# Kernel optimization log

Hardware: AMD Instinct MI355X
Metric: run time of the kernel (lower is better)

Reference implementation:

```python
import jax, jax.numpy as jnp
import numpy as np

N, E = 50000, 800000
NODE_IN, EDGE_IN, HID, OUT = 64, 16, 64, 32
BN_EPS = 1e-5


def _linear_params(key, fan_in, fan_out):
    kw, kb = jax.random.split(key)
    lim = 1.0 / np.sqrt(fan_in)
    W = jax.random.uniform(kw, (fan_in, fan_out), minval=-lim, maxval=lim, dtype=jnp.float32)
    b = jax.random.uniform(kb, (fan_out,), minval=-lim, maxval=lim, dtype=jnp.float32)
    return W, b


def setup_inputs() -> dict:
    key = jax.random.key(0)
    ks = jax.random.split(key, 8)
    x = jax.random.normal(ks[0], (N, NODE_IN), dtype=jnp.float32)
    edge_index = jax.random.randint(ks[1], (2, E), 0, N, dtype=jnp.int64)
    edge_attr = jax.random.normal(ks[2], (E, EDGE_IN), dtype=jnp.float32)
    # layer 1: message Linear(node_in + edge_in -> hid), self Linear(node_in -> hid)
    W1_msg, b1_msg = _linear_params(ks[3], NODE_IN + EDGE_IN, HID)
    W1_self, b1_self = _linear_params(ks[4], NODE_IN, HID)
    # BatchNorm1d(hidden) params (inference mode: running stats)
    bn_gamma = jnp.ones((HID,), jnp.float32)
    bn_beta = jnp.zeros((HID,), jnp.float32)
    bn_mean = jax.random.normal(ks[5], (HID,), dtype=jnp.float32) * 0.1
    bn_var = jax.random.uniform(ks[6], (HID,), minval=0.5, maxval=1.5, dtype=jnp.float32)
    # layer 2: message Linear(hid + edge_in -> out), self Linear(hid -> out)
    k7, k8 = jax.random.split(ks[7])
    W2_msg, b2_msg = _linear_params(k7, HID + EDGE_IN, OUT)
    W2_self, b2_self = _linear_params(k8, HID, OUT)
    return dict(x=x, edge_index=edge_index, edge_attr=edge_attr,
                W1_msg=W1_msg, b1_msg=b1_msg, W1_self=W1_self, b1_self=b1_self,
                bn_gamma=bn_gamma, bn_beta=bn_beta, bn_mean=bn_mean, bn_var=bn_var,
                W2_msg=W2_msg, b2_msg=b2_msg, W2_self=W2_self, b2_self=b2_self)


def _gnn_layer(x, edge_index, edge_attr, W_msg, b_msg, W_self, b_self):
    # gather source node features per edge, concat edge features, linear, scatter-sum to dst
    src, dst = edge_index[0], edge_index[1]
    m = jnp.concatenate([x[src], edge_attr], axis=-1) @ W_msg + b_msg  # [E, out]
    agg = jax.ops.segment_sum(m, dst, num_segments=x.shape[0])          # [N, out]
    return x @ W_self + b_self + agg


def reference(x, edge_index, edge_attr,
              W1_msg, b1_msg, W1_self, b1_self,
              bn_gamma, bn_beta, bn_mean, bn_var,
              W2_msg, b2_msg, W2_self, b2_self):
    h = _gnn_layer(x, edge_index, edge_attr, W1_msg, b1_msg, W1_self, b1_self)
    # BatchNorm1d (eval mode, running stats) + ReLU; dropout is identity in eval
    h = (h - bn_mean) * jax.lax.rsqrt(bn_var + BN_EPS) * bn_gamma + bn_beta
    h = jax.nn.relu(h)
    return _gnn_layer(h, edge_index, edge_attr, W2_msg, b2_msg, W2_self, b2_self)
```

## Files before the change

### kernel.cpp

```cpp
#include <hip/hip_runtime.h>

#define NN 50000
#define NE 800000
#define NB 6250
#define NT 3125
#define SCB 49
#define NBK 128
#define BNODE 391
#define BCAP 7680
#define SCAP 56

typedef __attribute__((ext_vector_type(8))) short short8x;
typedef __attribute__((ext_vector_type(4))) float f32x4;

#define OFF_CNT   0LL
#define OFF_ROW   ((long long)NN)
#define OFF_RECS  (3LL*NN + 16)
#define OFF_FLAGS (35LL*NN + 16)
#define OFF_BS    (35LL*NN + 32)
#define OFF_BO    (35LL*NN + 96)
#define OFF_PK    (35LL*NN + 160)
#define OFF_FB1S  (35LL*NN + 7840)
#define OFF_FB2S  (35LL*NN + 7904)
#define OFF_F1    (36LL*NN)
#define OFF_F2    (116LL*NN)
#define OFF_Y2B   (164LL*NN)
#define OFF_S2    (180LL*NN)
#define OFF_BCUR  (212LL*NN)

__device__ __forceinline__ float ldf(const void* p, long long i, int bf16) {
  if (bf16) {
    unsigned short u = ((const unsigned short*)p)[i];
    return __uint_as_float(((unsigned)u) << 16);
  }
  return ((const float*)p)[i];
}
__device__ __forceinline__ unsigned short f2bf(float f) {
  unsigned u = __float_as_uint(f);
  unsigned r = (u + 0x7fffu + ((u >> 16) & 1u)) >> 16;
  return (unsigned short)r;
}
__device__ __forceinline__ unsigned pk2(float lo, float hi) {
  return (unsigned)f2bf(lo) | ((unsigned)f2bf(hi) << 16);
}
__device__ __forceinline__ int ldidx(const void* p, long long i, int i64) {
  return i64 ? (int)((const long long*)p)[i] : ((const int*)p)[i];
}
__device__ __forceinline__ float bflo(unsigned u) { return __uint_as_float(u << 16); }
__device__ __forceinline__ float bfhi(unsigned u) { return __uint_as_float(u & 0xffff0000u); }

__global__ void k_detect(const void* ei, const void* x, int* flags) {
  int lane = threadIdx.x & 63;
  const int* p = (const int*)ei;
  int any = 0;
  for (int i = lane; i < 256; i += 64) any |= p[2 * i + 1];
  unsigned long long anyb = __ballot(any != 0);
  const unsigned short* q = (const unsigned short*)x;
  int cnt = 0;
  for (int i = lane; i < 256; i += 64) {
    unsigned short w = q[2 * i];
    int e = (w >> 7) & 0xff;
    if (w == 0 || (e >= 110 && e <= 140)) cnt++;
  }
  for (int m = 1; m < 64; m <<= 1) cnt += __shfl_xor(cnt, m, 64);
  if (lane == 0) {
    flags[0] = (anyb == 0ull) ? 1 : 0;
    flags[1] = (cnt >= 192) ? 1 : 0;
  }
}

__global__ __launch_bounds__(256) void k_prep(
    const void* __restrict__ W1_msg, const void* __restrict__ b1_msg,
    const void* __restrict__ W1_self, const void* __restrict__ b1_self,
    const void* __restrict__ gamma, const void* __restrict__ beta,
    const void* __restrict__ mean, const void* __restrict__ var,
    const void* __restrict__ W2_msg, const void* __restrict__ b2_msg,
    const void* __restrict__ W2_self, const void* __restrict__ b2_self,
    const int* __restrict__ flags, unsigned short* __restrict__ PK,
    float* __restrict__ fb1s, float* __restrict__ fb2s) {
  int bf = flags[1];
  int t0 = blockIdx.x * 256 + threadIdx.x;
  int stride = gridDim.x * 256;
  for (int i = t0; i < 10240; i += stride) {
    int j = i & 7, L = (i >> 3) & 63, t = (i >> 9) & 3, c = i >> 11;
    int k = c * 32 + ((L >> 4) << 3) + j;
    int col = t * 16 + (L & 15);
    float sc = ldf(gamma, col, bf) * rsqrtf(ldf(var, col, bf) + 1e-5f);
    float v;
    if (k < 64) v = ldf(W1_msg, k * 64 + col, bf) * sc;
    else if (k < 128) v = ldf(W1_self, (k - 64) * 64 + col, bf) * sc;
    else if (k < 144) v = ldf(W1_msg, (64 + k - 128) * 64 + col, bf) * sc;
    else if (k == 144) v = ldf(b1_msg, col, bf) * sc;
    else v = 0.0f;
    PK[i] = f2bf(v);
  }
  for (int i = t0; i < 2048; i += stride) {
    int j = i & 7, L = (i >> 3) & 63, t = (i >> 9) & 1, c = i >> 10;
    int k = c * 32 + ((L >> 4) << 3) + j;
    int col = t * 16 + (L & 15);
    PK[10240 + i] = f2bf(ldf(W2_msg, k * 32 + col, bf));
  }
  for (int i = t0; i < 3072; i += stride) {
    int j = i & 7, L = (i >> 3) & 63, t = (i >> 9) & 1, c = i >> 10;
    int k = c * 32 + ((L >> 4) << 3) + j;
    int col = t * 16 + (L & 15);
    float v;
    if (k < 64) v = ldf(W2_self, k * 32 + col, bf);
    else if (k < 80) v = ldf(W2_msg, k * 32 + col, bf);
    else if (k == 80) v = ldf(b2_msg, col, bf);
    else v = 0.0f;
    PK[12288 + i] = f2bf(v);
  }
  for (int i = t0; i < 64; i += stride) {
    float sc = ldf(gamma, i, bf) * rsqrtf(ldf(var, i, bf) + 1e-5f);
    fb1s[i] = ldf(b1_self, i, bf) * sc + ldf(beta, i, bf) - ldf(mean, i, bf) * sc;
  }
  for (int i = t0; i < 32; i += stride) fb2s[i] = ldf(b2_self, i, bf);
}

__global__ __launch_bounds__(256) void k_bin(const void* __restrict__ ei,
                                             const int* __restrict__ flags,
                                             int* __restrict__ bcur,
                                             int2* __restrict__ binbuf) {
  __shared__ int2 stage[NBK][SCAP];
  __shared__ int scnt[NBK];
  __shared__ int gbase[NBK];
  int tid = threadIdx.x;
  for (int i = tid; i < NBK; i += 256) scnt[i] = 0;
  __syncthreads();
  int i64 = flags[0];
  for (long long e0 = (long long)blockIdx.x * 256; e0 < NE;
       e0 += (long long)gridDim.x * 256) {
    long long e = e0 + tid;
    if (e < NE) {
      int src = ldidx(ei, e, i64);
      int dst = ldidx(ei, NE + e, i64);
      int b = dst / BNODE;
      int dl = dst - b * BNODE;
      int2 ent = make_int2(src | (dl << 16), (int)e);
      int pos = atomicAdd(&scnt[b], 1);
      if (pos < SCAP) {
        stage[b][pos] = ent;
      } else {
        int gp = atomicAdd(&bcur[b], 1);
        binbuf[(long long)b * BCAP + gp] = ent;
      }
    }
  }
  __syncthreads();
  if (tid < NBK) {
    int cb = scnt[tid] < SCAP ? scnt[tid] : SCAP;
    gbase[tid] = atomicAdd(&bcur[tid], cb);
  }
  __syncthreads();
  for (int b = 0; b < NBK; ++b) {
    int cb = scnt[b] < SCAP ? scnt[b] : SCAP;
    for (int i = tid; i < cb; i += 256)
      binbuf[(long long)b * BCAP + gbase[b] + i] = stage[b][i];
  }
}

__global__ __launch_bounds__(256) void k_bhist(const int* __restrict__ bcur,
                                               const int2* __restrict__ binbuf,
                                               int* __restrict__ counts) {
  __shared__ int lh[BNODE];
  int b = blockIdx.x;
  int tid = threadIdx.x;
  for (int i = tid; i < BNODE; i += 256) lh[i] = 0;
  __syncthreads();
  int cnt = bcur[b];
  for (int i = tid; i < cnt; i += 256) {
    int dl = (binbuf[(long long)b * BCAP + i].x >> 16) & 0x3FF;
    atomicAdd(&lh[dl], 1);
  }
  __syncthreads();
  int base = b * BNODE;
  int nn = NN - base < BNODE ? NN - base : BNODE;
  for (int i = tid; i < nn; i += 256) counts[base + i] = lh[i];
}

__global__ __launch_bounds__(1024) void k_scanA(const int* __restrict__ counts,
                                                int* __restrict__ bs) {
  __shared__ int sd[1024];
  int t = threadIdx.x;
  int i = blockIdx.x * 1024 + t;
  sd[t] = (i < NN) ? counts[i] : 0;
  __syncthreads();
  for (int off = 512; off > 0; off >>= 1) {
    if (t < off) sd[t] += sd[t + off];
    __syncthreads();
  }
  if (t == 0) bs[blockIdx.x] = sd[0];
}

__global__ void k_scanB(const int* __restrict__ bs, int* __restrict__ bo) {
  int lane = threadIdx.x & 63;
  int v = (lane < SCB) ? bs[lane] : 0;
  int orig = v;
  for (int off = 1; off < 64; off <<= 1) {
    int u = __shfl_up(v, off, 64);
    if (lane >= off) v += u;
  }
  if (lane < SCB) bo[lane] = v - orig;
}

__global__ __launch_bounds__(1024) void k_scanC(const int* __restrict__ counts,
                                                const int* __restrict__ bo,
                                                int* __restrict__ row_ptr) {
  __shared__ int sd[1024];
  int t = threadIdx.x;
  int i = blockIdx.x * 1024 + t;
  int v = (i < NN) ? counts[i] : 0;
  sd[t] = v;
  __syncthreads();
  for (int off = 1; off < 1024; off <<= 1) {
    int u = (t >= off) ? sd[t - off] : 0;
    __syncthreads();
    sd[t] += u;
    __syncthreads();
  }
  int excl = sd[t] - v + bo[blockIdx.x];
  if (i < NN) row_ptr[i] = excl;
  if (i == NN - 1) row_ptr[NN] = excl + v;
}

__global__ __launch_bounds__(256) void k_place(const int* __restrict__ bcur,
                                               const int2* __restrict__ binbuf,
                                               const int* __restrict__ row_ptr,
                                               int2* __restrict__ recs) {
  __shared__ int2 outb[BCAP];
  __shared__ int lcur[BNODE];
  int b = blockIdx.x;
  int tid = threadIdx.x;
  int base = b * BNODE;
  int nn = NN - base < BNODE ? NN - base : BNODE;
  int rbase = row_ptr[base];
  for (int i = tid; i < nn; i += 256) lcur[i] = row_ptr[base + i] - rbase;
  __syncthreads();
  int cnt = bcur[b];
  for (int i = tid; i < cnt; i += 256) {
    int2 ent = binbuf[(long long)b * BCAP + i];
    int dl = (ent.x >> 16) & 0x3FF;
    int p = atomicAdd(&lcur[dl], 1);
    outb[p] = make_int2(ent.x & 0xFFFF, ent.y);
  }
  __syncthreads();
  for (int i = tid; i < cnt; i += 256) recs[rbase + i] = outb[i];
}

__global__ __launch_bounds__(256) void k_gather1(
    const void* __restrict__ x, const void* __restrict__ ea,
    const int* __restrict__ row_ptr, const int2* __restrict__ recs,
    const int* __restrict__ flags, unsigned short* __restrict__ F1,
    unsigned short* __restrict__ F2) {
  int lane = threadIdx.x & 63;
  int g = lane >> 3, c = lane & 7;
  int bf = flags[1];
  long long wid = ((long long)blockIdx.x * blockDim.x + threadIdx.x) >> 6;
  long long nw = ((long long)gridDim.x * blockDim.x) >> 6;
  for (long long b = wid; b < NB; b += nw) {
    int n = (int)(b * 8 + g);
    int beg = row_ptr[n];
    int deg = row_ptr[n + 1] - beg;
    float a0 = 0.f, a1 = 0.f, a2 = 0.f, a3 = 0.f, a4 = 0.f, a5 = 0.f, a6 = 0.f, a7 = 0.f;
    float e0 = 0.f, e1 = 0.f, e2 = 0.f, e3 = 0.f;
    uint4 xw;
    if (bf) {
      const unsigned short* xs = (const unsigned short*)x;
      const unsigned short* es = (const unsigned short*)ea;
      int t = 0;
      for (; t + 4 <= deg; t += 4) {
        int2 r0 = recs[beg + t + 0];
        int2 r1 = recs[beg + t + 1];
        int2 r2 = recs[beg + t + 2];
        int2 r3 = recs[beg + t + 3];
        uint4 w0 = *((const uint4*)(xs + ((long long)r0.x << 6)) + c);
        uint4 w1 = *((const uint4*)(xs + ((long long)r1.x << 6)) + c);
        uint4 w2 = *((const uint4*)(xs + ((long long)r2.x << 6)) + c);
        uint4 w3 = *((const uint4*)(xs + ((long long)r3.x << 6)) + c);
        a0 += bflo(w0.x) + bflo(w1.x) + bflo(w2.x) + bflo(w3.x);
        a1 += bfhi(w0.x) + bfhi(w1.x) + bfhi(w2.x) + bfhi(w3.x);
        a2 += bflo(w0.y) + bflo(w1.y) + bflo(w2.y) + bflo(w3.y);
        a3 += bfhi(w0.y) + bfhi(w1.y) + bfhi(w2.y) + bfhi(w3.y);
        a4 += bflo(w0.z) + bflo(w1.z) + bflo(w2.z) + bflo(w3.z);
        a5 += bfhi(w0.z) + bfhi(w1.z) + bfhi(w2.z) + bfhi(w3.z);
        a6 += bflo(w0.w) + bflo(w1.w) + bflo(w2.w) + bflo(w3.w);
        a7 += bfhi(w0.w) + bfhi(w1.w) + bfhi(w2.w) + bfhi(w3.w);
        if (c < 4) {
          uint2 q0 = *((const uint2*)(es + ((long long)r0.y << 4)) + c);
          uint2 q1 = *((const uint2*)(es + ((long long)r1.y << 4)) + c);
          uint2 q2 = *((const uint2*)(es + ((long long)r2.y << 4)) + c);
          uint2 q3 = *((const uint2*)(es + ((long long)r3.y << 4)) + c);
          e0 += bflo(q0.x) + bflo(q1.x) + bflo(q2.x) + bflo(q3.x);
          e1 += bfhi(q0.x) + bfhi(q1.x) + bfhi(q2.x) + bfhi(q3.x);
          e2 += bflo(q0.y) + bflo(q1.y) + bflo(q2.y) + bflo(q3.y);
          e3 += bfhi(q0.y) + bfhi(q1.y) + bfhi(q2.y) + bfhi(q3.y);
        }
      }
      for (; t < deg; ++t) {
        int2 r = recs[beg + t];
        uint4 w = *((const uint4*)(xs + ((long long)r.x << 6)) + c);
        a0 += bflo(w.x); a1 += bfhi(w.x);
        a2 += bflo(w.y); a3 += bfhi(w.y);
        a4 += bflo(w.z); a5 += bfhi(w.z);
        a6 += bflo(w.w); a7 += bfhi(w.w);
        if (c < 4) {
          uint2 q = *((const uint2*)(es + ((long long)r.y << 4)) + c);
          e0 += bflo(q.x); e1 += bfhi(q.x);
          e2 += bflo(q.y); e3 += bfhi(q.y);
        }
      }
      xw = *((const uint4*)(xs + ((long long)n << 6)) + c);
    } else {
      const float* xf = (const float*)x;
      const float* ef = (const float*)ea;
      for (int t = 0; t < deg; ++t) {
        int2 r = recs[beg + t];
        float4 w0 = *((const float4*)(xf + ((long long)r.x << 6)) + c * 2);
        float4 w1 = *((const float4*)(xf + ((long long)r.x << 6)) + c * 2 + 1);
        a0 += w0.x; a1 += w0.y; a2 += w0.z; a3 += w0.w;
        a4 += w1.x; a5 += w1.y; a6 += w1.z; a7 += w1.w;
        if (c < 4) {
          float4 q = *((const float4*)(ef + ((long long)r.y << 4)) + c);
          e0 += q.x; e1 += q.y; e2 += q.z; e3 += q.w;
        }
      }
      float4 p0 = *((const float4*)(xf + ((long long)n << 6)) + c * 2);
      float4 p1 = *((const float4*)(xf + ((long long)n << 6)) + c * 2 + 1);
      xw = make_uint4(pk2(p0.x, p0.y), pk2(p0.z, p0.w), pk2(p1.x, p1.y), pk2(p1.z, p1.w));
    }
    unsigned short* f1 = F1 + (long long)n * 160;
    unsigned short* f2 = F2 + (long long)n * 96;
    *((uint4*)f1 + c) = make_uint4(pk2(a0, a1), pk2(a2, a3), pk2(a4, a5), pk2(a6, a7));
    *((uint4*)(f1 + 64) + c) = xw;
    if (c < 4) {
      uint2 sp = make_uint2(pk2(e0, e1), pk2(e2, e3));
      *((uint2*)(f1 + 128) + c) = sp;
      *((uint2*)(f2 + 64) + c) = sp;
    }
    if (c == 4) {
      unsigned d = (unsigned)f2bf((float)deg);
      *((uint4*)(f1 + 144)) = make_uint4(d, 0u, 0u, 0u);
      *((uint4*)(f2 + 80)) = make_uint4(d, 0u, 0u, 0u);
    }
    if (c == 5) {
      *((uint4*)(f1 + 152)) = make_uint4(0u, 0u, 0u, 0u);
      *((uint4*)(f2 + 88)) = make_uint4(0u, 0u, 0u, 0u);
    }
  }
}

__global__ __launch_bounds__(256) void k_gemm1(
    const unsigned short* __restrict__ F1, const unsigned short* __restrict__ PK,
    const float* __restrict__ fb1s, unsigned short* __restrict__ F2,
    unsigned short* __restrict__ Y2B) {
  __shared__ unsigned short hsh[4][16 * 72];
  int lane = threadIdx.x & 63;
  int wv = threadIdx.x >> 6;
  int m = lane & 15, quad = lane >> 4;
  unsigned short* hs = hsh[wv];
  short8x Bf[20];
#pragma unroll
  for (int s = 0; s < 20; ++s) Bf[s] = *(const short8x*)(PK + (s * 64 + lane) * 8);
  short8x By[4];
#pragma unroll
  for (int s = 0; s < 4; ++s) By[s] = *(const short8x*)(PK + 10240 + (s * 64 + lane) * 8);
  long long gw = (long long)blockIdx.x * 4 + wv;
  long long nw = (long long)gridDim.x * 4;
  for (long long tile = gw; tile < NT; tile += nw) {
    long long n0 = tile * 16;
    const unsigned short* f1 = F1 + (n0 + m) * 160 + quad * 8;
    short8x A[5];
#pragma unroll
    for (int cc = 0; cc < 5; ++cc) A[cc] = *(const short8x*)(f1 + cc * 32);
    f32x4 acc[4];
#pragma unroll
    for (int t = 0; t < 4; ++t) {
      float b = fb1s[t * 16 + m];
      acc[t] = (f32x4){b, b, b, b};
    }
#pragma unroll
    for (int cc = 0; cc < 5; ++cc) {
#pragma unroll
      for (int t = 0; t < 4; ++t)
        acc[t] = __builtin_amdgcn_mfma_f32_16x16x32_bf16(A[cc], Bf[cc * 4 + t], acc[t], 0, 0, 0);
    }
#pragma unroll
    for (int t = 0; t < 4; ++t) {
#pragma unroll
      for (int i = 0; i < 4; ++i) {
        float h = fmaxf(acc[t][i], 0.0f);
        unsigned short us = f2bf(h);
        F2[(n0 + quad * 4 + i) * 96 + t * 16 + m] = us;
        hs[(quad * 4 + i) * 72 + t * 16 + m] = us;
      }
    }
    __builtin_amdgcn_sched_barrier(0);
    f32x4 yacc[2];
    yacc[0] = (f32x4){0.f, 0.f, 0.f, 0.f};
    yacc[1] = (f32x4){0.f, 0.f, 0.f, 0.f};
#pragma unroll
    for (int cc = 0; cc < 2; ++cc) {
      short8x Ah = *(const short8x*)(hs + m * 72 + cc * 32 + quad * 8);
#pragma unroll
      for (int t = 0; t < 2; ++t)
        yacc[t] = __builtin_amdgcn_mfma_f32_16x16x32_bf16(Ah, By[cc * 2 + t], yacc[t], 0, 0, 0);
    }
#pragma unroll
    for (int t = 0; t < 2; ++t) {
#pragma unroll
      for (int i = 0; i < 4; ++i)
        Y2B[(n0 + quad * 4 + i) * 32 + t * 16 + m] = f2bf(yacc[t][i]);
    }
    __builtin_amdgcn_sched_barrier(0);
  }
}

__global__ __launch_bounds__(256) void k_gather2(
    const unsigned short* __restrict__ Y2B, const int* __restrict__ row_ptr,
    const int2* __restrict__ recs, float* __restrict__ S2) {
  int lane = threadIdx.x & 63;
  int g = lane >> 3, c = lane & 7;
  long long wid = ((long long)blockIdx.x * blockDim.x + threadIdx.x) >> 6;
  long long nw = ((long long)gridDim.x * blockDim.x) >> 6;
  for (long long b = wid; b < NB; b += nw) {
    int n = (int)(b * 8 + g);
    int beg = row_ptr[n];
    int deg = row_ptr[n + 1] - beg;
    float s0 = 0.f, s1 = 0.f, s2 = 0.f, s3 = 0.f;
    int t = 0;
    for (; t + 4 <= deg; t += 4) {
      int2 r0 = recs[beg + t + 0];
      int2 r1 = recs[beg + t + 1];
      int2 r2 = recs[beg + t + 2];
      int2 r3 = recs[beg + t + 3];
      uint2 q0 = *((const uint2*)(Y2B + (long long)r0.x * 32) + c);
      uint2 q1 = *((const uint2*)(Y2B + (long long)r1.x * 32) + c);
      uint2 q2 = *((const uint2*)(Y2B + (long long)r2.x * 32) + c);
      uint2 q3 = *((const uint2*)(Y2B + (long long)r3.x * 32) + c);
      s0 += bflo(q0.x) + bflo(q1.x) + bflo(q2.x) + bflo(q3.x);
      s1 += bfhi(q0.x) + bfhi(q1.x) + bfhi(q2.x) + bfhi(q3.x);
      s2 += bflo(q0.y) + bflo(q1.y) + bflo(q2.y) + bflo(q3.y);
      s3 += bfhi(q0.y) + bfhi(q1.y) + bfhi(q2.y) + bfhi(q3.y);
    }
    for (; t < deg; ++t) {
      int2 r = recs[beg + t];
      uint2 q = *((const uint2*)(Y2B + (long long)r.x * 32) + c);
      s0 += bflo(q.x); s1 += bfhi(q.x);
      s2 += bflo(q.y); s3 += bfhi(q.y);
    }
    *(float4*)(S2 + (long long)n * 32 + c * 4) = make_float4(s0, s1, s2, s3);
  }
}

__global__ __launch_bounds__(256) void k_gemm2(
    const unsigned short* __restrict__ F2, const unsigned short* __restrict__ PK,
    const float* __restrict__ fb2s, const float* __restrict__ S2,
    const int* __restrict__ flags, void* __restrict__ out) {
  int lane = threadIdx.x & 63;
  int wv = threadIdx.x >> 6;
  int m = lane & 15, quad = lane >> 4;
  int bf = flags[1];
  short8x Bf[6];
#pragma unroll
  for (int s = 0; s < 6; ++s) Bf[s] = *(const short8x*)(PK + 12288 + (s * 64 + lane) * 8);
  long long gw = (long long)blockIdx.x * 4 + wv;
  long long nw = (long long)gridDim.x * 4;
  for (long long tile = gw; tile < NT; tile += nw) {
    long long n0 = tile * 16;
    const unsigned short* f2 = F2 + (n0 + m) * 96 + quad * 8;
    short8x A[3];
#pragma unroll
    for (int cc = 0; cc < 3; ++cc) A[cc] = *(const short8x*)(f2 + cc * 32);
    f32x4 acc[2];
#pragma unroll
    for (int t = 0; t < 2; ++t) {
      float b = fb2s[t * 16 + m];
#pragma unroll
      for (int i = 0; i < 4; ++i)
        acc[t][i] = b + S2[(n0 + quad * 4 + i) * 32 + t * 16 + m];
    }
#pragma unroll
    for (int cc = 0; cc < 3; ++cc) {
#pragma unroll
      for (int t = 0; t < 2; ++t)
        acc[t] = __builtin_amdgcn_mfma_f32_16x16x32_bf16(A[cc], Bf[cc * 2 + t], acc[t], 0, 0, 0);
    }
#pragma unroll
    for (int t = 0; t < 2; ++t) {
#pragma unroll
      for (int i = 0; i < 4; ++i) {
        long long idx = (n0 + quad * 4 + i) * 32 + t * 16 + m;
        if (bf) ((unsigned short*)out)[idx] = f2bf(acc[t][i]);
        else ((float*)out)[idx] = acc[t][i];
      }
    }
  }
}

extern "C" void kernel_launch(void* const* d_in, const int* in_sizes, int n_in,
                              void* d_out, int out_size, void* d_ws, size_t ws_size,
                              hipStream_t stream) {
  const void* x = d_in[0];
  const void* ei = d_in[1];
  const void* ea = d_in[2];
  const void* W1_msg = d_in[3];
  const void* b1_msg = d_in[4];
  const void* W1_self = d_in[5];
  const void* b1_self = d_in[6];
  const void* gamma = d_in[7];
  const void* beta = d_in[8];
  const void* mean = d_in[9];
  const void* var = d_in[10];
  const void* W2_msg = d_in[11];
  const void* b2_msg = d_in[12];
  const void* W2_self = d_in[13];
  const void* b2_self = d_in[14];

  float* ws = (float*)d_ws;
  int* counts = (int*)(ws + OFF_CNT);
  int* row_ptr = (int*)(ws + OFF_ROW);
  int2* recs = (int2*)(ws + OFF_RECS);
  int* flags = (int*)(ws + OFF_FLAGS);
  int* bs = (int*)(ws + OFF_BS);
  int* bo = (int*)(ws + OFF_BO);
  unsigned short* PK = (unsigned short*)(ws + OFF_PK);
  float* fb1s = ws + OFF_FB1S;
  float* fb2s = ws + OFF_FB2S;
  unsigned short* F1 = (unsigned short*)(ws + OFF_F1);
  int2* binbuf = (int2*)(ws + OFF_F1);
  unsigned short* F2 = (unsigned short*)(ws + OFF_F2);
  unsigned short* Y2B = (unsigned short*)(ws + OFF_Y2B);
  float* S2 = ws + OFF_S2;
  int* bcur = (int*)(ws + OFF_BCUR);

  hipLaunchKernelGGL(k_detect, dim3(1), dim3(64), 0, stream, ei, x, flags);
  hipMemsetAsync(bcur, 0, NBK * sizeof(int), stream);
  hipLaunchKernelGGL(k_prep, dim3(64), dim3(256), 0, stream, W1_msg, b1_msg, W1_self,
                     b1_self, gamma, beta, mean, var, W2_msg, b2_msg, W2_self, b2_self,
                     flags, PK, fb1s, fb2s);

  hipLaunchKernelGGL(k_bin, dim3(256), dim3(256), 0, stream, ei, flags, bcur, binbuf);
  hipLaunchKernelGGL(k_bhist, dim3(NBK), dim3(256), 0, stream, bcur, binbuf, counts);
  hipLaunchKernelGGL(k_scanA, dim3(SCB), dim3(1024), 0, stream, counts, bs);
  hipLaunchKernelGGL(k_scanB, dim3(1), dim3(64), 0, stream, bs, bo);
  hipLaunchKernelGGL(k_scanC, dim3(SCB), dim3(1024), 0, stream, counts, bo, row_ptr);
  hipLaunchKernelGGL(k_place, dim3(NBK), dim3(256), 0, stream, bcur, binbuf, row_ptr,
                     recs);

  int gblocks = (NB + 3) / 4;
  hipLaunchKernelGGL(k_gather1, dim3(gblocks), dim3(256), 0, stream, x, ea, row_ptr,
                     recs, flags, F1, F2);
  int mblocks = (NT + 3) / 4;
  hipLaunchKernelGGL(k_gemm1, dim3(mblocks), dim3(256), 0, stream, F1, PK, fb1s, F2,
                     Y2B);
  hipLaunchKernelGGL(k_gather2, dim3(gblocks), dim3(256), 0, stream, Y2B, row_ptr, recs,
                     S2);
  hipLaunchKernelGGL(k_gemm2, dim3(mblocks), dim3(256), 0, stream, F2, PK, fb2s, S2,
                     flags, d_out);
}
```

Baseline: 246.6 us.

## Sort nodes by in-degree so gather waves process similar-degree nodes

```diff
diff --git a/kernel.cpp b/kernel.cpp
--- a/kernel.cpp
+++ b/kernel.cpp
@@ -27,6 +27,9 @@
 #define OFF_Y2B   (164LL*NN)
 #define OFF_S2    (180LL*NN)
 #define OFF_BCUR  (212LL*NN)
+#define OFF_DH    (212LL*NN + 128)
+#define OFF_DOFF  (212LL*NN + 256)
+#define OFF_PERM  (212LL*NN + 384)
 
 __device__ __forceinline__ float ldf(const void* p, long long i, int bf16) {
   if (bf16) {
@@ -162,7 +165,8 @@
 
 __global__ __launch_bounds__(256) void k_bhist(const int* __restrict__ bcur,
                                                const int2* __restrict__ binbuf,
-                                               int* __restrict__ counts) {
+                                               int* __restrict__ counts,
+                                               int* __restrict__ deghist) {
   __shared__ int lh[BNODE];
   int b = blockIdx.x;
   int tid = threadIdx.x;
@@ -176,7 +180,38 @@
   __syncthreads();
   int base = b * BNODE;
   int nn = NN - base < BNODE ? NN - base : BNODE;
-  for (int i = tid; i < nn; i += 256) counts[base + i] = lh[i];
+  for (int i = tid; i < nn; i += 256) {
+    int d = lh[i];
+    counts[base + i] = d;
+    atomicAdd(&deghist[d > 127 ? 127 : d], 1);
+  }
+}
+
+__global__ void k_dscan(const int* __restrict__ dh, int* __restrict__ doff) {
+  __shared__ int s[128];
+  int t = threadIdx.x;
+  int orig = dh[t];
+  s[t] = orig;
+  __syncthreads();
+  for (int off = 1; off < 128; off <<= 1) {
+    int u = (t + off < 128) ? s[t + off] : 0;
+    __syncthreads();
+    s[t] += u;
+    __syncthreads();
+  }
+  doff[t] = s[t] - orig;
+}
+
+__global__ __launch_bounds__(256) void k_perm(const int* __restrict__ counts,
+                                              int* __restrict__ doff,
+                                              int* __restrict__ perm) {
+  int n = blockIdx.x * 256 + threadIdx.x;
+  if (n < NN) {
+    int d = counts[n];
+    if (d > 127) d = 127;
+    int pos = atomicAdd(&doff[d], 1);
+    perm[pos] = n;
+  }
 }
 
 __global__ __launch_bounds__(1024) void k_scanA(const int* __restrict__ counts,
@@ -251,15 +286,15 @@
 __global__ __launch_bounds__(256) void k_gather1(
     const void* __restrict__ x, const void* __restrict__ ea,
     const int* __restrict__ row_ptr, const int2* __restrict__ recs,
-    const int* __restrict__ flags, unsigned short* __restrict__ F1,
-    unsigned short* __restrict__ F2) {
+    const int* __restrict__ perm, const int* __restrict__ flags,
+    unsigned short* __restrict__ F1, unsigned short* __restrict__ F2) {
   int lane = threadIdx.x & 63;
   int g = lane >> 3, c = lane & 7;
   int bf = flags[1];
   long long wid = ((long long)blockIdx.x * blockDim.x + threadIdx.x) >> 6;
   long long nw = ((long long)gridDim.x * blockDim.x) >> 6;
   for (long long b = wid; b < NB; b += nw) {
-    int n = (int)(b * 8 + g);
+    int n = perm[(int)(b * 8) + g];
     int beg = row_ptr[n];
     int deg = row_ptr[n + 1] - beg;
     float a0 = 0.f, a1 = 0.f, a2 = 0.f, a3 = 0.f, a4 = 0.f, a5 = 0.f, a6 = 0.f, a7 = 0.f;
@@ -418,13 +453,14 @@
 
 __global__ __launch_bounds__(256) void k_gather2(
     const unsigned short* __restrict__ Y2B, const int* __restrict__ row_ptr,
-    const int2* __restrict__ recs, float* __restrict__ S2) {
+    const int2* __restrict__ recs, const int* __restrict__ perm,
+    float* __restrict__ S2) {
   int lane = threadIdx.x & 63;
   int g = lane >> 3, c = lane & 7;
   long long wid = ((long long)blockIdx.x * blockDim.x + threadIdx.x) >> 6;
   long long nw = ((long long)gridDim.x * blockDim.x) >> 6;
   for (long long b = wid; b < NB; b += nw) {
-    int n = (int)(b * 8 + g);
+    int n = perm[(int)(b * 8) + g];
     int beg = row_ptr[n];
     int deg = row_ptr[n + 1] - beg;
     float s0 = 0.f, s1 = 0.f, s2 = 0.f, s3 = 0.f;
@@ -533,15 +569,22 @@
   unsigned short* Y2B = (unsigned short*)(ws + OFF_Y2B);
   float* S2 = ws + OFF_S2;
   int* bcur = (int*)(ws + OFF_BCUR);
+  int* deghist = (int*)(ws + OFF_DH);
+  int* doff = (int*)(ws + OFF_DOFF);
+  int* perm = (int*)(ws + OFF_PERM);
 
   hipLaunchKernelGGL(k_detect, dim3(1), dim3(64), 0, stream, ei, x, flags);
-  hipMemsetAsync(bcur, 0, NBK * sizeof(int), stream);
+  hipMemsetAsync(bcur, 0, 256 * sizeof(int), stream);
   hipLaunchKernelGGL(k_prep, dim3(64), dim3(256), 0, stream, W1_msg, b1_msg, W1_self,
                      b1_self, gamma, beta, mean, var, W2_msg, b2_msg, W2_self, b2_self,
                      flags, PK, fb1s, fb2s);
 
   hipLaunchKernelGGL(k_bin, dim3(256), dim3(256), 0, stream, ei, flags, bcur, binbuf);
-  hipLaunchKernelGGL(k_bhist, dim3(NBK), dim3(256), 0, stream, bcur, binbuf, counts);
+  hipLaunchKernelGGL(k_bhist, dim3(NBK), dim3(256), 0, stream, bcur, binbuf, counts,
+                     deghist);
+  hipLaunchKernelGGL(k_dscan, dim3(1), dim3(128), 0, stream, deghist, doff);
+  hipLaunchKernelGGL(k_perm, dim3((NN + 255) / 256), dim3(256), 0, stream, counts, doff,
+                     perm);
   hipLaunchKernelGGL(k_scanA, dim3(SCB), dim3(1024), 0, stream, counts, bs);
   hipLaunchKernelGGL(k_scanB, dim3(1), dim3(64), 0, stream, bs, bo);
   hipLaunchKernelGGL(k_scanC, dim3(SCB), dim3(1024), 0, stream, counts, bo, row_ptr);
@@ -550,12 +593,12 @@
 
   int gblocks = (NB + 3) / 4;
   hipLaunchKernelGGL(k_gather1, dim3(gblocks), dim3(256), 0, stream, x, ea, row_ptr,
-                     recs, flags, F1, F2);
+                     recs, perm, flags, F1, F2);
   int mblocks = (NT + 3) / 4;
   hipLaunchKernelGGL(k_gemm1, dim3(mblocks), dim3(256), 0, stream, F1, PK, fb1s, F2,
                      Y2B);
   hipLaunchKernelGGL(k_gather2, dim3(gblocks), dim3(256), 0, stream, Y2B, row_ptr, recs,
-                     S2);
+                     perm, S2);
   hipLaunchKernelGGL(k_gemm2, dim3(mblocks), dim3(256), 0, stream, F2, PK, fb2s, S2,
                      flags, d_out);
 }
```

Result: slower. 521.6 us (+111.5%).

## Fuse bin histogram and node scan into placement kernel, scan bin totals only

Applied to the files above, without the earlier changes.

```diff
diff --git a/kernel.cpp b/kernel.cpp
--- a/kernel.cpp
+++ b/kernel.cpp
@@ -4,7 +4,6 @@
 #define NE 800000
 #define NB 6250
 #define NT 3125
-#define SCB 49
 #define NBK 128
 #define BNODE 391
 #define BCAP 7680
@@ -19,9 +18,9 @@
 #define OFF_FLAGS (35LL*NN + 16)
 #define OFF_BS    (35LL*NN + 32)
 #define OFF_BO    (35LL*NN + 96)
-#define OFF_PK    (35LL*NN + 160)
-#define OFF_FB1S  (35LL*NN + 7840)
-#define OFF_FB2S  (35LL*NN + 7904)
+#define OFF_PK    (35LL*NN + 256)
+#define OFF_FB1S  (35LL*NN + 7936)
+#define OFF_FB2S  (35LL*NN + 8000)
 #define OFF_F1    (36LL*NN)
 #define OFF_F2    (116LL*NN)
 #define OFF_Y2B   (164LL*NN)
@@ -160,84 +159,65 @@
   }
 }
 
-__global__ __launch_bounds__(256) void k_bhist(const int* __restrict__ bcur,
-                                               const int2* __restrict__ binbuf,
-                                               int* __restrict__ counts) {
-  __shared__ int lh[BNODE];
-  int b = blockIdx.x;
-  int tid = threadIdx.x;
-  for (int i = tid; i < BNODE; i += 256) lh[i] = 0;
-  __syncthreads();
-  int cnt = bcur[b];
-  for (int i = tid; i < cnt; i += 256) {
-    int dl = (binbuf[(long long)b * BCAP + i].x >> 16) & 0x3FF;
-    atomicAdd(&lh[dl], 1);
-  }
-  __syncthreads();
-  int base = b * BNODE;
-  int nn = NN - base < BNODE ? NN - base : BNODE;
-  for (int i = tid; i < nn; i += 256) counts[base + i] = lh[i];
-}
-
-__global__ __launch_bounds__(1024) void k_scanA(const int* __restrict__ counts,
-                                                int* __restrict__ bs) {
-  __shared__ int sd[1024];
+__global__ void k_scan128(const int* __restrict__ bcur, int* __restrict__ bo) {
+  __shared__ int s[NBK];
   int t = threadIdx.x;
-  int i = blockIdx.x * 1024 + t;
-  sd[t] = (i < NN) ? counts[i] : 0;
-  __syncthreads();
-  for (int off = 512; off > 0; off >>= 1) {
-    if (t < off) sd[t] += sd[t + off];
+  int orig = bcur[t];
+  s[t] = orig;
+  __syncthreads();
+  for (int off = 1; off < NBK; off <<= 1) {
+    int u = (t >= off) ? s[t - off] : 0;
     __syncthreads();
-  }
-  if (t == 0) bs[blockIdx.x] = sd[0];
-}
-
-__global__ void k_scanB(const int* __restrict__ bs, int* __restrict__ bo) {
-  int lane = threadIdx.x & 63;
-  int v = (lane < SCB) ? bs[lane] : 0;
-  int orig = v;
-  for (int off = 1; off < 64; off <<= 1) {
-    int u = __shfl_up(v, off, 64);
-    if (lane >= off) v += u;
-  }
-  if (lane < SCB) bo[lane] = v - orig;
-}
-
-__global__ __launch_bounds__(1024) void k_scanC(const int* __restrict__ counts,
-                                                const int* __restrict__ bo,
-                                                int* __restrict__ row_ptr) {
-  __shared__ int sd[1024];
-  int t = threadIdx.x;
-  int i = blockIdx.x * 1024 + t;
-  int v = (i < NN) ? counts[i] : 0;
-  sd[t] = v;
-  __syncthreads();
-  for (int off = 1; off < 1024; off <<= 1) {
-    int u = (t >= off) ? sd[t - off] : 0;
+    s[t] += u;
     __syncthreads();
-    sd[t] += u;
-    __syncthreads();
-  }
-  int excl = sd[t] - v + bo[blockIdx.x];
-  if (i < NN) row_ptr[i] = excl;
-  if (i == NN - 1) row_ptr[NN] = excl + v;
+  }
+  bo[t] = s[t] - orig;
 }
 
 __global__ __launch_bounds__(256) void k_place(const int* __restrict__ bcur,
                                                const int2* __restrict__ binbuf,
-                                               const int* __restrict__ row_ptr,
+                                               const int* __restrict__ bo,
+                                               int* __restrict__ row_ptr,
                                                int2* __restrict__ recs) {
   __shared__ int2 outb[BCAP];
+  __shared__ int lh[BNODE];
+  __shared__ int lexc[BNODE];
   __shared__ int lcur[BNODE];
   int b = blockIdx.x;
   int tid = threadIdx.x;
   int base = b * BNODE;
   int nn = NN - base < BNODE ? NN - base : BNODE;
-  int rbase = row_ptr[base];
-  for (int i = tid; i < nn; i += 256) lcur[i] = row_ptr[base + i] - rbase;
-  __syncthreads();
   int cnt = bcur[b];
+  int rbase = bo[b];
+  for (int i = tid; i < BNODE; i += 256) lh[i] = 0;
+  __syncthreads();
+  for (int i = tid; i < cnt; i += 256) {
+    int dl = (binbuf[(long long)b * BCAP + i].x >> 16) & 0x3FF;
+    atomicAdd(&lh[dl], 1);
+  }
+  __syncthreads();
+  if (tid < 64) {
+    int carry = 0;
+    for (int c0 = 0; c0 < BNODE; c0 += 64) {
+      int i = c0 + tid;
+      int orig = (i < nn) ? lh[i] : 0;
+      int v = orig;
+      for (int off = 1; off < 64; off <<= 1) {
+        int u = __shfl_up(v, off, 64);
+        if (tid >= off) v += u;
+      }
+      if (i < nn) lexc[i] = carry + v - orig;
+      carry += __shfl(v, 63, 64);
+    }
+  }
+  __syncthreads();
+  for (int i = tid; i < nn; i += 256) {
+    int e = lexc[i];
+    row_ptr[base + i] = rbase + e;
+    lcur[i] = e;
+  }
+  if (b == NBK - 1 && tid == 0) row_ptr[NN] = rbase + cnt;
+  __syncthreads();
   for (int i = tid; i < cnt; i += 256) {
     int2 ent = binbuf[(long long)b * BCAP + i];
     int dl = (ent.x >> 16) & 0x3FF;
@@ -518,11 +498,9 @@
   const void* b2_self = d_in[14];
 
   float* ws = (float*)d_ws;
-  int* counts = (int*)(ws + OFF_CNT);
   int* row_ptr = (int*)(ws + OFF_ROW);
   int2* recs = (int2*)(ws + OFF_RECS);
   int* flags = (int*)(ws + OFF_FLAGS);
-  int* bs = (int*)(ws + OFF_BS);
   int* bo = (int*)(ws + OFF_BO);
   unsigned short* PK = (unsigned short*)(ws + OFF_PK);
   float* fb1s = ws + OFF_FB1S;
@@ -541,12 +519,9 @@
                      flags, PK, fb1s, fb2s);
 
   hipLaunchKernelGGL(k_bin, dim3(256), dim3(256), 0, stream, ei, flags, bcur, binbuf);
-  hipLaunchKernelGGL(k_bhist, dim3(NBK), dim3(256), 0, stream, bcur, binbuf, counts);
-  hipLaunchKernelGGL(k_scanA, dim3(SCB), dim3(1024), 0, stream, counts, bs);
-  hipLaunchKernelGGL(k_scanB, dim3(1), dim3(64), 0, stream, bs, bo);
-  hipLaunchKernelGGL(k_scanC, dim3(SCB), dim3(1024), 0, stream, counts, bo, row_ptr);
-  hipLaunchKernelGGL(k_place, dim3(NBK), dim3(256), 0, stream, bcur, binbuf, row_ptr,
-                     recs);
+  hipLaunchKernelGGL(k_scan128, dim3(1), dim3(NBK), 0, stream, bcur, bo);
+  hipLaunchKernelGGL(k_place, dim3(NBK), dim3(256), 0, stream, bcur, binbuf, bo,
+                     row_ptr, recs);
 
   int gblocks = (NB + 3) / 4;
   hipLaunchKernelGGL(k_gather1, dim3(gblocks), dim3(256), 0, stream, x, ea, row_ptr,
```

Result: faster. 241.4 us (-2.1%).
